# Optimization experiments

Measured on AMD Instinct MI355X. Metric: run time of the kernel, lower is better.

Reference implementation:

```python
import jax, jax.numpy as jnp
import numpy as np

B, T, H = 4096, 2048, 64  # batch, max seq len, hidden size
IN = 1                    # decoder input hardcoded to width 1 in source
BOT = 3                   # latent bottleneck (linear_enc: H->3, linear_dec: 3->H)


def setup_inputs() -> dict:
    key = jax.random.key(0)
    ks = jax.random.split(key, 16)
    s = 1.0 / np.sqrt(H)
    u = lambda k, shape: jax.random.uniform(k, shape, jnp.float32, -s, s)
    padded = jax.random.normal(ks[0], (B, T, IN), jnp.float32)
    seq_lengths = jax.random.randint(ks[1], (B,), 1, T + 1).at[0].set(T)  # max == T (static unroll)
    return {
        "padded": padded,
        "seq_lengths": seq_lengths,
        # encoder LSTM (gate order i,f,g,o like torch); biases b_ih+b_hh fused
        "enc_Wih": u(ks[2], (4 * H, IN)),
        "enc_Whh": u(ks[3], (4 * H, H)),
        "enc_b":   u(ks[4], (4 * H,)),
        # encoder bottleneck linear H->3
        "enc_linW": u(ks[5], (BOT, H)),
        "enc_linb": u(ks[6], (BOT,)),
        # decoder expand linear 3->H
        "dec_linW": u(ks[7], (H, BOT)),
        "dec_linb": u(ks[8], (H,)),
        # decoder LSTM
        "dec_Wih": u(ks[9], (4 * H, IN)),
        "dec_Whh": u(ks[10], (4 * H, H)),
        "dec_b":   u(ks[11], (4 * H,)),
        # output linear H->1
        "outW": u(ks[12], (IN, H)),
        "outb": u(ks[13], (IN,)),
    }


def _lstm_cell(x, h, c, Wih, Whh, b):
    g = x @ Wih.T + h @ Whh.T + b
    i, f, gg, o = jnp.split(g, 4, axis=-1)
    c = jax.nn.sigmoid(f) * c + jax.nn.sigmoid(i) * jnp.tanh(gg)
    h = jax.nn.sigmoid(o) * jnp.tanh(c)
    return h, c


def reference(padded, seq_lengths, enc_Wih, enc_Whh, enc_b, enc_linW, enc_linb,
              dec_linW, dec_linb, dec_Wih, dec_Whh, dec_b, outW, outb):
    Bn, Tn, _ = padded.shape
    Hn = enc_Whh.shape[1]
    xs = jnp.transpose(padded, (1, 0, 2))                       # (T, B, 1)
    mask = jnp.arange(Tn)[:, None] < seq_lengths[None, :]        # (T, B)

    # ---- encoder: packed semantics == freeze (h,c) past each seq's length ----
    h0 = jnp.zeros((Bn, Hn), padded.dtype)
    def enc_step(carry, xm):
        h, c = carry
        x, m = xm
        nh, nc = _lstm_cell(x, h, c, enc_Wih, enc_Whh, enc_b)
        m = m[:, None]
        return (jnp.where(m, nh, h), jnp.where(m, nc, c)), None
    (h, c), _ = jax.lax.scan(enc_step, (h0, h0), (xs, mask))

    hz = jax.nn.sigmoid(h @ enc_linW.T + enc_linb)               # (B, 3) latent

    hd = hz @ dec_linW.T + dec_linb                              # (B, H)
    x0 = jnp.zeros((Bn, 1), padded.dtype)
    def dec_step(carry, _):
        x, hh, cc = carry
        nh, nc = _lstm_cell(x, hh, cc, dec_Wih, dec_Whh, dec_b)
        y = nh @ outW.T + outb
        return (y, nh, nc), y
    _, ys = jax.lax.scan(dec_step, (x0, hd, c), None, length=Tn)  # (T, B, 1)
    output = jnp.transpose(ys, (1, 0, 2))                         # (B, T, 1)

    # ---- masked MSE ----
    maskf = mask.T[:, :, None].astype(padded.dtype)               # (B, T, 1)
    loss = (((padded - output) ** 2) * maskf).sum() / maskf.sum()
    return loss, padded, output, hz[None]
```

## Files before the change

### kernel.cpp

```cpp
#include <hip/hip_runtime.h>

#define B 4096
#define T 2048
#define H 64
#define NBATCH 16
#define NB (B / NBATCH)
#define NTHREADS 512

typedef __attribute__((ext_vector_type(8))) short short8;
typedef __attribute__((ext_vector_type(4))) float f32x4;

__device__ __forceinline__ float ex2(float x) { return __builtin_amdgcn_exp2f(x); }
__device__ __forceinline__ float sigm(float x) {
    return __builtin_amdgcn_rcpf(1.0f + ex2(-1.4426950408889634f * x));
}
__device__ __forceinline__ float tanh_(float x) {
    float xc = fminf(15.0f, fmaxf(-15.0f, x));
    float e = ex2(2.8853900817779268f * xc);
    return (e - 1.0f) * __builtin_amdgcn_rcpf(e + 1.0f);
}
__device__ __forceinline__ unsigned short f2bf(float f) {
    unsigned u = __builtin_bit_cast(unsigned, f);
    u += 0x7fffu + ((u >> 16) & 1u);
    return (unsigned short)(u >> 16);
}
__device__ __forceinline__ void lds_barrier() {
    asm volatile("s_waitcnt lgkmcnt(0)\n\ts_barrier" ::: "memory");
}

extern "C" __global__ void __launch_bounds__(NTHREADS, 2)
enc_kernel(const float* __restrict__ padded, const int* __restrict__ seq_len,
           const float* __restrict__ Wih, const float* __restrict__ Whh,
           const float* __restrict__ bias,
           float* __restrict__ h_out, float* __restrict__ c_out)
{
    __shared__ unsigned short hA[2][NBATCH][72];
    __shared__ int slen[NBATCH];

    const int tid = threadIdx.x;
    const int w = tid >> 6, L = tid & 63, lo = L & 15, hi = L >> 4;
    const int b0 = blockIdx.x * NBATCH;

    short8 af[2][2];
    #pragma unroll
    for (int tt = 0; tt < 2; ++tt) {
        const int G = (lo & 3) * 64 + (2 * w + tt) * 4 + (lo >> 2);
        #pragma unroll
        for (int kk = 0; kk < 2; ++kk) {
            const float* src = Whh + (long)G * H + kk * 32 + hi * 8;
            short8 f;
            #pragma unroll
            for (int j = 0; j < 8; ++j) f[j] = (short)f2bf(src[j]);
            af[tt][kk] = f;
        }
    }
    float b_g[2][4], wi_g[2][4];
    #pragma unroll
    for (int tt = 0; tt < 2; ++tt)
        #pragma unroll
        for (int r = 0; r < 4; ++r) {
            const int G2 = r * 64 + (2 * w + tt) * 4 + hi;
            b_g[tt][r] = bias[G2];
            wi_g[tt][r] = Wih[G2];
        }

    for (int i = tid; i < NBATCH * 64; i += NTHREADS) hA[0][i >> 6][i & 63] = 0;
    if (tid < NBATCH) slen[tid] = seq_len[b0 + tid];
    lds_barrier();

    int maxlen = 1;
    #pragma unroll
    for (int i = 0; i < NBATCH; ++i) maxlen = max(maxlen, slen[i]);
    const int len_lo = slen[lo];

    const float* xrow = padded + (long)(b0 + lo) * T;
    f32x4 xc = *(const f32x4*)(xrow);
    f32x4 xn = *(const f32x4*)(xrow + 4);

    float c_st[2] = {0, 0}, h_st[2] = {0, 0};
    const int u_unit0 = 8 * w + hi, u_unit1 = 8 * w + 4 + hi;

#define ESTEP(P, XI)                                                          \
    {                                                                         \
        const float x = xc[XI];                                               \
        short8 hb0 = *(const short8*)&hA[P][lo][hi * 8];                      \
        short8 hb1 = *(const short8*)&hA[P][lo][32 + hi * 8];                 \
        f32x4 acc[2];                                                         \
        _Pragma("unroll")                                                     \
        for (int tt = 0; tt < 2; ++tt) {                                      \
            f32x4 z = {b_g[tt][0] + wi_g[tt][0] * x,                          \
                       b_g[tt][1] + wi_g[tt][1] * x,                          \
                       b_g[tt][2] + wi_g[tt][2] * x,                          \
                       b_g[tt][3] + wi_g[tt][3] * x};                         \
            z = __builtin_amdgcn_mfma_f32_16x16x32_bf16(af[tt][0], hb0, z, 0,0,0);       \
            acc[tt] = __builtin_amdgcn_mfma_f32_16x16x32_bf16(af[tt][1], hb1, z, 0,0,0); \
        }                                                                     \
        const bool act = (t + XI) < len_lo;                                   \
        _Pragma("unroll")                                                     \
        for (int tt = 0; tt < 2; ++tt) {                                      \
            float i_ = sigm(acc[tt][0]);                                      \
            float f_ = sigm(acc[tt][1]);                                      \
            float g_ = tanh_(acc[tt][2]);                                     \
            float o_ = sigm(acc[tt][3]);                                      \
            float cn = f_ * c_st[tt] + i_ * g_;                               \
            float hn = o_ * tanh_(cn);                                        \
            if (act) { c_st[tt] = cn; h_st[tt] = hn; }                        \
        }                                                                     \
        hA[(P) ^ 1][lo][u_unit0] = f2bf(h_st[0]);                             \
        hA[(P) ^ 1][lo][u_unit1] = f2bf(h_st[1]);                             \
        lds_barrier();                                                        \
    }

    for (int t = 0; t < maxlen; t += 4) {
        int nb = t + 8; if (nb > T - 4) nb = T - 4;
        f32x4 xf = *(const f32x4*)(xrow + nb);
        ESTEP(0, 0) ESTEP(1, 1) ESTEP(0, 2) ESTEP(1, 3)
        xc = xn; xn = xf;
    }
#undef ESTEP

    h_out[(long)(b0 + lo) * H + u_unit0] = h_st[0];
    h_out[(long)(b0 + lo) * H + u_unit1] = h_st[1];
    c_out[(long)(b0 + lo) * H + u_unit0] = c_st[0];
    c_out[(long)(b0 + lo) * H + u_unit1] = c_st[1];
}

extern "C" __global__ void __launch_bounds__(256)
mid_kernel(const float* __restrict__ h_enc,
           const float* __restrict__ eW, const float* __restrict__ eb,
           const float* __restrict__ dW, const float* __restrict__ db,
           const float* __restrict__ outW, const float* __restrict__ outb,
           float* __restrict__ hz_out, float* __restrict__ hd_out,
           float* __restrict__ y0c)
{
    int b = blockIdx.x * blockDim.x + threadIdx.x;
    if (b >= B) return;
    const float* h = h_enc + (long)b * H;
    float hz[3];
    #pragma unroll
    for (int j = 0; j < 3; ++j) {
        float s = eb[j];
        for (int k = 0; k < H; ++k) s += h[k] * eW[j*H + k];
        hz[j] = sigm(s);
        hz_out[b*3 + j] = hz[j];
    }
    float y0 = outb[0];
    for (int u = 0; u < H; ++u) {
        float hd = db[u] + hz[0]*dW[u*3] + hz[1]*dW[u*3+1] + hz[2]*dW[u*3+2];
        hd_out[(long)b*H + u] = hd;
        y0 += outW[u] * hd;
    }
    y0c[b] = y0;
}

extern "C" __global__ void __launch_bounds__(NTHREADS, 2)
dec_kernel(const float* __restrict__ hd, const float* __restrict__ c_in,
           const float* __restrict__ Wih, const float* __restrict__ Whh,
           const float* __restrict__ bias, const float* __restrict__ outW,
           const float* __restrict__ outb, const float* __restrict__ y0c,
           float* __restrict__ y_out)
{
    __shared__ unsigned short hA[2][NBATCH][72];

    const int tid = threadIdx.x;
    const int w = tid >> 6, L = tid & 63, lo = L & 15, hi = L >> 4;
    const int b0 = blockIdx.x * NBATCH;

    short8 af[2][2];
    #pragma unroll
    for (int tt = 0; tt < 2; ++tt) {
        const int G = (lo & 3) * 64 + (2 * w + tt) * 4 + (lo >> 2);
        const float wir = Wih[G];
        #pragma unroll
        for (int kk = 0; kk < 2; ++kk) {
            const float* src = Whh + (long)G * H + kk * 32 + hi * 8;
            const float* ow  = outW + kk * 32 + hi * 8;
            short8 f;
            #pragma unroll
            for (int j = 0; j < 8; ++j) f[j] = (short)f2bf(src[j] + wir * ow[j]);
            af[tt][kk] = f;
        }
    }
    const float outb_s = outb[0];
    const float y0 = y0c[b0 + lo];
    float b_g[2][4], corr[2][4];
    #pragma unroll
    for (int tt = 0; tt < 2; ++tt)
        #pragma unroll
        for (int r = 0; r < 4; ++r) {
            const int G2 = r * 64 + (2 * w + tt) * 4 + hi;
            const float wir = Wih[G2];
            b_g[tt][r] = bias[G2] + wir * outb_s;
            corr[tt][r] = wir * y0;
        }
    short8 ya[2] = { (short8)0, (short8)0 };
    if (w == 0 && lo == 0) {
        #pragma unroll
        for (int kk = 0; kk < 2; ++kk) {
            short8 f;
            #pragma unroll
            for (int j = 0; j < 8; ++j) f[j] = (short)f2bf(outW[kk*32 + hi*8 + j]);
            ya[kk] = f;
        }
    }

    for (int i = tid; i < NBATCH * 64; i += NTHREADS) {
        int m = i >> 6, k = i & 63;
        hA[0][m][k] = f2bf(hd[(long)(b0 + m) * H + k]);
    }
    const int u_unit0 = 8 * w + hi, u_unit1 = 8 * w + 4 + hi;
    float c_st[2];
    c_st[0] = c_in[(long)(b0 + lo) * H + u_unit0];
    c_st[1] = c_in[(long)(b0 + lo) * H + u_unit1];
    lds_barrier();

#define DSTEP(P, CORR, TT)                                                    \
    {                                                                         \
        short8 hb0 = *(const short8*)&hA[P][lo][hi * 8];                      \
        short8 hb1 = *(const short8*)&hA[P][lo][32 + hi * 8];                 \
        f32x4 acc[2];                                                         \
        _Pragma("unroll")                                                     \
        for (int tt = 0; tt < 2; ++tt) {                                      \
            f32x4 z = {b_g[tt][0], b_g[tt][1], b_g[tt][2], b_g[tt][3]};       \
            z = __builtin_amdgcn_mfma_f32_16x16x32_bf16(af[tt][0], hb0, z, 0,0,0);       \
            acc[tt] = __builtin_amdgcn_mfma_f32_16x16x32_bf16(af[tt][1], hb1, z, 0,0,0); \
        }                                                                     \
        if (w == 0) {   \
            f32x4 zy = {outb_s, outb_s, outb_s, outb_s};                      \
            zy = __builtin_amdgcn_mfma_f32_16x16x32_bf16(ya[0], hb0, zy, 0,0,0); \
            zy = __builtin_amdgcn_mfma_f32_16x16x32_bf16(ya[1], hb1, zy, 0,0,0); \
            if ((TT) > 0 && hi == 0)                                          \
                y_out[(long)(b0 + lo) * T + ((TT) - 1)] = zy[0];              \
        }                                                                     \
        if (CORR) {                                                           \
            _Pragma("unroll")                                                 \
            for (int tt = 0; tt < 2; ++tt)                                    \
                _Pragma("unroll")                                             \
                for (int r = 0; r < 4; ++r) acc[tt][r] -= corr[tt][r];        \
        }                                                                     \
        _Pragma("unroll")                                                     \
        for (int tt = 0; tt < 2; ++tt) {                                      \
            float i_ = sigm(acc[tt][0]);                                      \
            float f_ = sigm(acc[tt][1]);                                      \
            float g_ = tanh_(acc[tt][2]);                                     \
            float o_ = sigm(acc[tt][3]);                                      \
            float cn = f_ * c_st[tt] + i_ * g_;                               \
            float hn = o_ * tanh_(cn);                                        \
            c_st[tt] = cn;                                                    \
            hA[(P) ^ 1][lo][tt ? u_unit1 : u_unit0] = f2bf(hn);               \
        }                                                                     \
        lds_barrier();                                                        \
    }

    DSTEP(0, 1, 0) DSTEP(1, 0, 1) DSTEP(0, 0, 2) DSTEP(1, 0, 3)
    for (int t = 4; t < T; t += 4) {
        DSTEP(0, 0, t) DSTEP(1, 0, t + 1) DSTEP(0, 0, t + 2) DSTEP(1, 0, t + 3)
    }
#undef DSTEP

    if (w == 0) {
        short8 hb0 = *(const short8*)&hA[0][lo][hi * 8];
        short8 hb1 = *(const short8*)&hA[0][lo][32 + hi * 8];
        f32x4 zy = {outb_s, outb_s, outb_s, outb_s};
        zy = __builtin_amdgcn_mfma_f32_16x16x32_bf16(ya[0], hb0, zy, 0,0,0);
        zy = __builtin_amdgcn_mfma_f32_16x16x32_bf16(ya[1], hb1, zy, 0,0,0);
        if (hi == 0) y_out[(long)(b0 + lo) * T + (T - 1)] = zy[0];
    }
}

extern "C" __global__ void __launch_bounds__(256)
loss_kernel(const float* __restrict__ padded, const float* __restrict__ y,
            const int* __restrict__ seq_len, float* __restrict__ acc2)
{
    const long n4 = (long)B * T / 4;
    long i0 = (long)(blockIdx.x * blockDim.x + threadIdx.x);
    long stride = (long)gridDim.x * blockDim.x;
    float s = 0.f, cnt = 0.f;
    for (long i = i0; i < n4; i += stride) {
        int b = (int)(i >> 9);
        int t = (int)(i & 511) * 4;
        int len = seq_len[b];
        f32x4 pv = *(const f32x4*)&padded[i * 4];
        f32x4 yv = *(const f32x4*)&y[i * 4];
        #pragma unroll
        for (int e = 0; e < 4; ++e)
            if (t + e < len) { float d = pv[e] - yv[e]; s += d * d; cnt += 1.0f; }
    }
    for (int m = 1; m < 64; m <<= 1) { s += __shfl_xor(s, m); cnt += __shfl_xor(cnt, m); }
    if ((threadIdx.x & 63) == 0) { atomicAdd(&acc2[0], s); atomicAdd(&acc2[1], cnt); }
}

extern "C" __global__ void fin_kernel(const float* __restrict__ acc2, float* __restrict__ out)
{
    out[0] = acc2[0] / acc2[1];
}

extern "C" void kernel_launch(void* const* d_in, const int* in_sizes, int n_in,
                              void* d_out, int out_size, void* d_ws, size_t ws_size,
                              hipStream_t stream)
{
    const float* padded = (const float*)d_in[0];
    const int*   seq    = (const int*)  d_in[1];
    const float* eWih   = (const float*)d_in[2];
    const float* eWhh   = (const float*)d_in[3];
    const float* eb     = (const float*)d_in[4];
    const float* elW    = (const float*)d_in[5];
    const float* elb    = (const float*)d_in[6];
    const float* dlW    = (const float*)d_in[7];
    const float* dlb    = (const float*)d_in[8];
    const float* dWih   = (const float*)d_in[9];
    const float* dWhh   = (const float*)d_in[10];
    const float* db     = (const float*)d_in[11];
    const float* outW   = (const float*)d_in[12];
    const float* outb   = (const float*)d_in[13];
    float* out = (float*)d_out;

    float* ws    = (float*)d_ws;
    float* h_enc = ws;
    float* c_enc = ws + (long)B * H;
    float* hd    = ws + 2L * B * H;
    float* y0c   = ws + 3L * B * H;
    float* acc2  = ws + 3L * B * H + B;

    float* out_pad = out + 1;
    float* out_y   = out + 1 + (long)B * T;
    float* out_hz  = out + 1 + 2L * (long)B * T;

    hipMemcpyAsync(out_pad, padded, (long)B * T * sizeof(float),
                   hipMemcpyDeviceToDevice, stream);
    hipMemsetAsync(acc2, 0, 2 * sizeof(float), stream);

    enc_kernel<<<NB, NTHREADS, 0, stream>>>(padded, seq, eWih, eWhh, eb, h_enc, c_enc);
    mid_kernel<<<B / 256, 256, 0, stream>>>(h_enc, elW, elb, dlW, dlb, outW, outb,
                                            out_hz, hd, y0c);
    dec_kernel<<<NB, NTHREADS, 0, stream>>>(hd, c_enc, dWih, dWhh, db, outW, outb, y0c, out_y);
    loss_kernel<<<1024, 256, 0, stream>>>(padded, out_y, seq, acc2);
    fin_kernel<<<1, 1, 0, stream>>>(acc2, out);
}
```

Baseline: 2.084 ms.

## Double threads per block so each wave handles one gate tile

Blocks grow from 512 to 1024 threads (16 waves), so each wave computes one 16-unit gate tile per step instead of two. This halves per-wave MFMA and activation work on the serial recurrent critical path, at the cost of a 16-wave barrier each step and one block per CU. The decoder's output-projection MFMA rotates across waves by time step instead of always running on wave 0, spreading that extra work.

```diff
diff --git a/kernel.cpp b/kernel.cpp
--- a/kernel.cpp
+++ b/kernel.cpp
@@ -5,7 +5,7 @@
 #define H 64
 #define NBATCH 16
 #define NB (B / NBATCH)
-#define NTHREADS 512
+#define NTHREADS 1024
 
 typedef __attribute__((ext_vector_type(8))) short short8;
 typedef __attribute__((ext_vector_type(4))) float f32x4;
@@ -28,7 +28,7 @@
     asm volatile("s_waitcnt lgkmcnt(0)\n\ts_barrier" ::: "memory");
 }
 
-extern "C" __global__ void __launch_bounds__(NTHREADS, 2)
+extern "C" __global__ void __launch_bounds__(NTHREADS, 1)
 enc_kernel(const float* __restrict__ padded, const int* __restrict__ seq_len,
            const float* __restrict__ Wih, const float* __restrict__ Whh,
            const float* __restrict__ bias,
@@ -40,31 +40,29 @@
     const int tid = threadIdx.x;
     const int w = tid >> 6, L = tid & 63, lo = L & 15, hi = L >> 4;
     const int b0 = blockIdx.x * NBATCH;
-
-    short8 af[2][2];
-    #pragma unroll
-    for (int tt = 0; tt < 2; ++tt) {
-        const int G = (lo & 3) * 64 + (2 * w + tt) * 4 + (lo >> 2);
+    const int unit = w * 4 + hi;
+
+    short8 af[2];
+    {
+        const int G = (lo & 3) * 64 + w * 4 + (lo >> 2);
         #pragma unroll
         for (int kk = 0; kk < 2; ++kk) {
             const float* src = Whh + (long)G * H + kk * 32 + hi * 8;
             short8 f;
             #pragma unroll
             for (int j = 0; j < 8; ++j) f[j] = (short)f2bf(src[j]);
-            af[tt][kk] = f;
+            af[kk] = f;
         }
     }
-    float b_g[2][4], wi_g[2][4];
-    #pragma unroll
-    for (int tt = 0; tt < 2; ++tt)
-        #pragma unroll
-        for (int r = 0; r < 4; ++r) {
-            const int G2 = r * 64 + (2 * w + tt) * 4 + hi;
-            b_g[tt][r] = bias[G2];
-            wi_g[tt][r] = Wih[G2];
-        }
-
-    for (int i = tid; i < NBATCH * 64; i += NTHREADS) hA[0][i >> 6][i & 63] = 0;
+    float b_g[4], wi_g[4];
+    #pragma unroll
+    for (int r = 0; r < 4; ++r) {
+        const int G2 = r * 64 + unit;
+        b_g[r] = bias[G2];
+        wi_g[r] = Wih[G2];
+    }
+
+    if (tid < NBATCH * 64) hA[0][tid >> 6][tid & 63] = 0;
     if (tid < NBATCH) slen[tid] = seq_len[b0 + tid];
     lds_barrier();
 
@@ -77,37 +75,26 @@
     f32x4 xc = *(const f32x4*)(xrow);
     f32x4 xn = *(const f32x4*)(xrow + 4);
 
-    float c_st[2] = {0, 0}, h_st[2] = {0, 0};
-    const int u_unit0 = 8 * w + hi, u_unit1 = 8 * w + 4 + hi;
+    float c_st = 0.f, h_st = 0.f;
 
 #define ESTEP(P, XI)                                                          \
     {                                                                         \
         const float x = xc[XI];                                               \
         short8 hb0 = *(const short8*)&hA[P][lo][hi * 8];                      \
         short8 hb1 = *(const short8*)&hA[P][lo][32 + hi * 8];                 \
-        f32x4 acc[2];                                                         \
-        _Pragma("unroll")                                                     \
-        for (int tt = 0; tt < 2; ++tt) {                                      \
-            f32x4 z = {b_g[tt][0] + wi_g[tt][0] * x,                          \
-                       b_g[tt][1] + wi_g[tt][1] * x,                          \
-                       b_g[tt][2] + wi_g[tt][2] * x,                          \
-                       b_g[tt][3] + wi_g[tt][3] * x};                         \
-            z = __builtin_amdgcn_mfma_f32_16x16x32_bf16(af[tt][0], hb0, z, 0,0,0);       \
-            acc[tt] = __builtin_amdgcn_mfma_f32_16x16x32_bf16(af[tt][1], hb1, z, 0,0,0); \
-        }                                                                     \
+        f32x4 z = {b_g[0] + wi_g[0] * x, b_g[1] + wi_g[1] * x,                \
+                   b_g[2] + wi_g[2] * x, b_g[3] + wi_g[3] * x};               \
+        z = __builtin_amdgcn_mfma_f32_16x16x32_bf16(af[0], hb0, z, 0,0,0);    \
+        f32x4 acc = __builtin_amdgcn_mfma_f32_16x16x32_bf16(af[1], hb1, z, 0,0,0); \
         const bool act = (t + XI) < len_lo;                                   \
-        _Pragma("unroll")                                                     \
-        for (int tt = 0; tt < 2; ++tt) {                                      \
-            float i_ = sigm(acc[tt][0]);                                      \
-            float f_ = sigm(acc[tt][1]);                                      \
-            float g_ = tanh_(acc[tt][2]);                                     \
-            float o_ = sigm(acc[tt][3]);                                      \
-            float cn = f_ * c_st[tt] + i_ * g_;                               \
-            float hn = o_ * tanh_(cn);                                        \
-            if (act) { c_st[tt] = cn; h_st[tt] = hn; }                        \
-        }                                                                     \
-        hA[(P) ^ 1][lo][u_unit0] = f2bf(h_st[0]);                             \
-        hA[(P) ^ 1][lo][u_unit1] = f2bf(h_st[1]);                             \
+        float i_ = sigm(acc[0]);                                              \
+        float f_ = sigm(acc[1]);                                              \
+        float g_ = tanh_(acc[2]);                                             \
+        float o_ = sigm(acc[3]);                                              \
+        float cn = f_ * c_st + i_ * g_;                                       \
+        float hn = o_ * tanh_(cn);                                            \
+        if (act) { c_st = cn; h_st = hn; }                                    \
+        hA[(P) ^ 1][lo][unit] = f2bf(h_st);                                   \
         lds_barrier();                                                        \
     }
 
@@ -119,10 +106,8 @@
     }
 #undef ESTEP
 
-    h_out[(long)(b0 + lo) * H + u_unit0] = h_st[0];
-    h_out[(long)(b0 + lo) * H + u_unit1] = h_st[1];
-    c_out[(long)(b0 + lo) * H + u_unit0] = c_st[0];
-    c_out[(long)(b0 + lo) * H + u_unit1] = c_st[1];
+    h_out[(long)(b0 + lo) * H + unit] = h_st;
+    c_out[(long)(b0 + lo) * H + unit] = c_st;
 }
 
 extern "C" __global__ void __launch_bounds__(256)
@@ -153,7 +138,7 @@
     y0c[b] = y0;
 }
 
-extern "C" __global__ void __launch_bounds__(NTHREADS, 2)
+extern "C" __global__ void __launch_bounds__(NTHREADS, 1)
 dec_kernel(const float* __restrict__ hd, const float* __restrict__ c_in,
            const float* __restrict__ Wih, const float* __restrict__ Whh,
            const float* __restrict__ bias, const float* __restrict__ outW,
@@ -165,11 +150,11 @@
     const int tid = threadIdx.x;
     const int w = tid >> 6, L = tid & 63, lo = L & 15, hi = L >> 4;
     const int b0 = blockIdx.x * NBATCH;
-
-    short8 af[2][2];
-    #pragma unroll
-    for (int tt = 0; tt < 2; ++tt) {
-        const int G = (lo & 3) * 64 + (2 * w + tt) * 4 + (lo >> 2);
+    const int unit = w * 4 + hi;
+
+    short8 af[2];
+    {
+        const int G = (lo & 3) * 64 + w * 4 + (lo >> 2);
         const float wir = Wih[G];
         #pragma unroll
         for (int kk = 0; kk < 2; ++kk) {
@@ -178,54 +163,44 @@
             short8 f;
             #pragma unroll
             for (int j = 0; j < 8; ++j) f[j] = (short)f2bf(src[j] + wir * ow[j]);
-            af[tt][kk] = f;
+            af[kk] = f;
         }
     }
     const float outb_s = outb[0];
     const float y0 = y0c[b0 + lo];
-    float b_g[2][4], corr[2][4];
-    #pragma unroll
-    for (int tt = 0; tt < 2; ++tt)
-        #pragma unroll
-        for (int r = 0; r < 4; ++r) {
-            const int G2 = r * 64 + (2 * w + tt) * 4 + hi;
-            const float wir = Wih[G2];
-            b_g[tt][r] = bias[G2] + wir * outb_s;
-            corr[tt][r] = wir * y0;
-        }
-    short8 ya[2] = { (short8)0, (short8)0 };
-    if (w == 0 && lo == 0) {
-        #pragma unroll
-        for (int kk = 0; kk < 2; ++kk) {
-            short8 f;
+    float b_g[4], corr[4];
+    #pragma unroll
+    for (int r = 0; r < 4; ++r) {
+        const int G2 = r * 64 + unit;
+        const float wir = Wih[G2];
+        b_g[r] = bias[G2] + wir * outb_s;
+        corr[r] = wir * y0;
+    }
+    short8 ya[2];
+    #pragma unroll
+    for (int kk = 0; kk < 2; ++kk) {
+        short8 f = (short8)0;
+        if (lo == 0)
             #pragma unroll
             for (int j = 0; j < 8; ++j) f[j] = (short)f2bf(outW[kk*32 + hi*8 + j]);
-            ya[kk] = f;
-        }
-    }
-
-    for (int i = tid; i < NBATCH * 64; i += NTHREADS) {
-        int m = i >> 6, k = i & 63;
+        ya[kk] = f;
+    }
+
+    if (tid < NBATCH * 64) {
+        int m = tid >> 6, k = tid & 63;
         hA[0][m][k] = f2bf(hd[(long)(b0 + m) * H + k]);
     }
-    const int u_unit0 = 8 * w + hi, u_unit1 = 8 * w + 4 + hi;
-    float c_st[2];
-    c_st[0] = c_in[(long)(b0 + lo) * H + u_unit0];
-    c_st[1] = c_in[(long)(b0 + lo) * H + u_unit1];
+    float c_st = c_in[(long)(b0 + lo) * H + unit];
     lds_barrier();
 
 #define DSTEP(P, CORR, TT)                                                    \
     {                                                                         \
         short8 hb0 = *(const short8*)&hA[P][lo][hi * 8];                      \
         short8 hb1 = *(const short8*)&hA[P][lo][32 + hi * 8];                 \
-        f32x4 acc[2];                                                         \
-        _Pragma("unroll")                                                     \
-        for (int tt = 0; tt < 2; ++tt) {                                      \
-            f32x4 z = {b_g[tt][0], b_g[tt][1], b_g[tt][2], b_g[tt][3]};       \
-            z = __builtin_amdgcn_mfma_f32_16x16x32_bf16(af[tt][0], hb0, z, 0,0,0);       \
-            acc[tt] = __builtin_amdgcn_mfma_f32_16x16x32_bf16(af[tt][1], hb1, z, 0,0,0); \
-        }                                                                     \
-        if (w == 0) {   \
+        f32x4 z = {b_g[0], b_g[1], b_g[2], b_g[3]};                           \
+        z = __builtin_amdgcn_mfma_f32_16x16x32_bf16(af[0], hb0, z, 0,0,0);    \
+        f32x4 acc = __builtin_amdgcn_mfma_f32_16x16x32_bf16(af[1], hb1, z, 0,0,0); \
+        if (w == ((TT) & 15)) {     \
             f32x4 zy = {outb_s, outb_s, outb_s, outb_s};                      \
             zy = __builtin_amdgcn_mfma_f32_16x16x32_bf16(ya[0], hb0, zy, 0,0,0); \
             zy = __builtin_amdgcn_mfma_f32_16x16x32_bf16(ya[1], hb1, zy, 0,0,0); \
@@ -234,21 +209,16 @@
         }                                                                     \
         if (CORR) {                                                           \
             _Pragma("unroll")                                                 \
-            for (int tt = 0; tt < 2; ++tt)                                    \
-                _Pragma("unroll")                                             \
-                for (int r = 0; r < 4; ++r) acc[tt][r] -= corr[tt][r];        \
+            for (int r = 0; r < 4; ++r) acc[r] -= corr[r];                    \
         }                                                                     \
-        _Pragma("unroll")                                                     \
-        for (int tt = 0; tt < 2; ++tt) {                                      \
-            float i_ = sigm(acc[tt][0]);                                      \
-            float f_ = sigm(acc[tt][1]);                                      \
-            float g_ = tanh_(acc[tt][2]);                                     \
-            float o_ = sigm(acc[tt][3]);                                      \
-            float cn = f_ * c_st[tt] + i_ * g_;                               \
-            float hn = o_ * tanh_(cn);                                        \
-            c_st[tt] = cn;                                                    \
-            hA[(P) ^ 1][lo][tt ? u_unit1 : u_unit0] = f2bf(hn);               \
-        }                                                                     \
+        float i_ = sigm(acc[0]);                                              \
+        float f_ = sigm(acc[1]);                                              \
+        float g_ = tanh_(acc[2]);                                             \
+        float o_ = sigm(acc[3]);                                              \
+        float cn = f_ * c_st + i_ * g_;                                       \
+        float hn = o_ * tanh_(cn);                                            \
+        c_st = cn;                                                            \
+        hA[(P) ^ 1][lo][unit] = f2bf(hn);                                     \
         lds_barrier();                                                        \
     }
 
```

Result: faster. 2.001 ms (-4.0%).
